# Performance work log

Measured on AMD Instinct MI355X. Metric: run time of the kernel, lower is better.

The kernel has to match this reference:

```python
import jax, jax.numpy as jnp
import numpy as np

D_MODEL, N_HEADS, HEAD_DIM = 384, 12, 32
N_QP, N_VP = 4, 8
B, L = 2, 1024
OUT_DIM = N_HEADS * (HEAD_DIM + N_VP * 3 + N_VP)  # 12*(32+24+8)=768
LN_EPS = 1e-5


def _linear_params(key, din, dout):
    kw, _ = jax.random.split(key)
    W = jax.random.normal(kw, (din, dout), dtype=jnp.float32) / np.sqrt(din).astype(np.float32)
    b = jnp.zeros((dout,), dtype=jnp.float32)
    return W, b


def setup_inputs() -> dict:
    key = jax.random.key(0)
    ks = jax.random.split(key, 12)
    s = jax.random.normal(ks[0], (B, L, D_MODEL), dtype=jnp.float32)
    translations = jax.random.normal(ks[1], (B, L, 3), dtype=jnp.float32)
    # proper rotation-ish matrices via QR of random gaussians
    g = jax.random.normal(ks[2], (B, L, 3, 3), dtype=jnp.float32)
    rotations, _ = jnp.linalg.qr(g)
    mask = jnp.ones((B, L), dtype=bool)
    Wq, bq = _linear_params(ks[3], D_MODEL, N_HEADS * HEAD_DIM)
    Wk, bk = _linear_params(ks[4], D_MODEL, N_HEADS * HEAD_DIM)
    Wv, bv = _linear_params(ks[5], D_MODEL, N_HEADS * HEAD_DIM)
    Wqp, bqp = _linear_params(ks[6], D_MODEL, N_HEADS * N_QP * 3)
    Wkp, bkp = _linear_params(ks[7], D_MODEL, N_HEADS * N_QP * 3)
    Wvp, bvp = _linear_params(ks[8], D_MODEL, N_HEADS * N_VP * 3)
    Wo, bo = _linear_params(ks[9], OUT_DIM, D_MODEL)
    head_weights = jnp.zeros((N_HEADS,), dtype=jnp.float32)
    ln_g = jnp.ones((D_MODEL,), dtype=jnp.float32)
    ln_b = jnp.zeros((D_MODEL,), dtype=jnp.float32)
    return dict(s=s, translations=translations, rotations=rotations, mask=mask,
                ln_g=ln_g, ln_b=ln_b, Wq=Wq, bq=bq, Wk=Wk, bk=bk, Wv=Wv, bv=bv,
                Wqp=Wqp, bqp=bqp, Wkp=Wkp, bkp=bkp, Wvp=Wvp, bvp=bvp,
                head_weights=head_weights, Wo=Wo, bo=bo)


def _ipa(s, translations, rotations, mask, ln_g, ln_b, Wq, bq, Wk, bk, Wv, bv,
         Wqp, bqp, Wkp, bkp, Wvp, bvp, head_weights, Wo, bo):
    Bc, Lc, _ = s.shape
    # LayerNorm
    mu = jnp.mean(s, axis=-1, keepdims=True)
    var = jnp.mean((s - mu) ** 2, axis=-1, keepdims=True)
    h = (s - mu) * jax.lax.rsqrt(var + LN_EPS) * ln_g + ln_b

    q_s = (h @ Wq + bq).reshape(Bc, Lc, N_HEADS, HEAD_DIM)
    k_s = (h @ Wk + bk).reshape(Bc, Lc, N_HEADS, HEAD_DIM)
    v_s = (h @ Wv + bv).reshape(Bc, Lc, N_HEADS, HEAD_DIM)
    q_pts = (h @ Wqp + bqp).reshape(Bc, Lc, N_HEADS, N_QP, 3)
    k_pts = (h @ Wkp + bkp).reshape(Bc, Lc, N_HEADS, N_QP, 3)
    v_pts = (h @ Wvp + bvp).reshape(Bc, Lc, N_HEADS, N_VP, 3)

    T = translations[:, :, None, None, :]  # (B,L,1,1,3)
    # local -> global: out_d = sum_c p_c R_{cd}  (matches torch einsum 'blhpc,blhpcd')
    q_g = jnp.einsum('blhpc,blcd->blhpd', q_pts, rotations) + T
    k_g = jnp.einsum('blhpc,blcd->blhpd', k_pts, rotations) + T
    v_g = jnp.einsum('blhpc,blcd->blhpd', v_pts, rotations) + T

    scalar_attn = jnp.einsum('bihd,bjhd->bhij', q_s, k_s) / np.sqrt(HEAD_DIM).astype(np.float32)

    # sum_{p,c} (q_i - k_j)^2 = |q_i|^2 + |k_j|^2 - 2 q_i.k_j  (avoids B,H,L,L,P,3 tensor)
    q2 = jnp.einsum('bihpc,bihpc->bhi', q_g, q_g)
    k2 = jnp.einsum('bjhpc,bjhpc->bhj', k_g, k_g)
    cross = jnp.einsum('bihpc,bjhpc->bhij', q_g, k_g)
    pt_dists = q2[:, :, :, None] + k2[:, :, None, :] - 2.0 * cross  # (B,H,L,L)

    w_h = jax.nn.softplus(head_weights)[None, :, None, None]
    attn_logits = scalar_attn - 0.5 * w_h * pt_dists
    attn_logits = jnp.where(mask[:, None, None, :], attn_logits, -jnp.inf)
    attn = jax.nn.softmax(attn_logits, axis=-1)  # (B,H,L,L)

    result_scalar = jnp.einsum('bhij,bjhd->bihd', attn, v_s).reshape(Bc, Lc, N_HEADS * HEAD_DIM)
    result_pts = jnp.einsum('bhij,bjhpc->bihpc', attn, v_g)  # (B,L,H,VP,3)
    # global -> local with R^T: out_d = sum_c x_c (R^T)_{cd} = sum_c x_c R_{dc}
    result_pts_local = jnp.einsum('blhpc,bldc->blhpd', result_pts - T, rotations)
    result_pts_norm = jnp.sqrt(jnp.sum(result_pts_local ** 2, axis=-1))  # (B,L,H,VP)

    output = jnp.concatenate([
        result_scalar,
        result_pts_local.reshape(Bc, Lc, N_HEADS * N_VP * 3),
        result_pts_norm.reshape(Bc, Lc, N_HEADS * N_VP),
    ], axis=-1)
    return s + output @ Wo + bo


def reference(s, translations, rotations, mask, ln_g, ln_b, Wq, bq, Wk, bk, Wv, bv,
              Wqp, bqp, Wkp, bkp, Wvp, bvp, head_weights, Wo, bo):
    return _ipa(s, translations, rotations, mask, ln_g, ln_b, Wq, bq, Wk, bk, Wv, bv,
                Wqp, bqp, Wkp, bkp, Wvp, bvp, head_weights, Wo, bo)
```

## Files before the change

kernel.cpp:

```cpp
#include <hip/hip_runtime.h>
#include <hip/hip_bf16.h>

constexpr int B_ = 2, L_ = 1024, D_ = 384, H_ = 12, HD_ = 32;
constexpr int NQP = 4, NVP = 8;
constexpr int ROWS = B_ * L_;
constexpr int PROJ_N = 1728;
constexpr int OUTD = 768;
constexpr int KAUG = 48;
constexpr int C_QS = 0, C_KS = 384, C_VS = 768, C_QP = 1152, C_KP = 1296, C_VP = 1440;

constexpr size_t OFF_HH   = 0;
constexpr size_t OFF_HL   = OFF_HH   + (size_t)ROWS * D_ / 2;
constexpr size_t OFF_WTH  = OFF_HL   + (size_t)ROWS * D_ / 2;
constexpr size_t OFF_WTL  = OFF_WTH  + (size_t)PROJ_N * D_ / 2;
constexpr size_t OFF_BC   = OFF_WTL  + (size_t)PROJ_N * D_ / 2;
constexpr size_t OFF_P    = OFF_BC   + PROJ_N;
constexpr size_t OFF_QPK  = OFF_P    + (size_t)ROWS * PROJ_N;
constexpr size_t QP_FL    = (size_t)24 * 1024 * KAUG / 2;
constexpr size_t OFF_QPL  = OFF_QPK  + QP_FL;
constexpr size_t OFF_KPK  = OFF_QPL  + QP_FL;
constexpr size_t OFF_KPL2 = OFF_KPK  + QP_FL;
constexpr size_t OFF_VT   = OFF_KPL2 + (size_t)24 * 1024 * 16 / 2;
constexpr size_t OFF_OH   = OFF_VT   + (size_t)24 * 64 * L_ / 2;
constexpr size_t OFF_WOH  = OFF_OH   + (size_t)ROWS * OUTD / 2;

typedef __attribute__((ext_vector_type(8)))  __bf16        bf16x8;
typedef __attribute__((ext_vector_type(16))) float         f32x16;
typedef __attribute__((ext_vector_type(4)))  unsigned int  u32x4;
typedef __attribute__((ext_vector_type(8)))  unsigned short us8;

__device__ __forceinline__ unsigned short f2bf(float x) {
    unsigned u = __builtin_bit_cast(unsigned, x);
    unsigned r = (u + 0x7FFFu + ((u >> 16) & 1u)) >> 16;
    return (unsigned short)r;
}
__device__ __forceinline__ float bf2f(unsigned short s) {
    return __builtin_bit_cast(float, (unsigned)s << 16);
}

#define MFMA(a, b, c) __builtin_amdgcn_mfma_f32_32x32x16_bf16((a), (b), (c), 0, 0, 0)
#define CVTPK(dst, x, y) asm("v_cvt_pk_bf16_f32 %0, %1, %2" : "=v"(dst) : "v"(x), "v"(y))
#define PSWAP(a, b) asm("v_permlane32_swap_b32 %0, %1" : "+v"(a), "+v"(b))

typedef const __attribute__((address_space(1))) void* gas_cp;
typedef __attribute__((address_space(3))) void* las_p;
__device__ __forceinline__ void gload16(const void* g, void* l) {
    __builtin_amdgcn_global_load_lds((gas_cp)g, (las_p)l, 16, 0, 0);
}

__global__ __launch_bounds__(256) void setup_kernel(
    const float* __restrict__ s, const float* __restrict__ g,
    const float* __restrict__ bln,
    const float* __restrict__ Wq, const float* __restrict__ Wk, const float* __restrict__ Wv,
    const float* __restrict__ Wqp, const float* __restrict__ Wkp, const float* __restrict__ Wvp,
    const float* __restrict__ bq, const float* __restrict__ bk, const float* __restrict__ bv,
    const float* __restrict__ bqp, const float* __restrict__ bkp, const float* __restrict__ bvp,
    const float* __restrict__ Wo,
    unsigned short* __restrict__ Hhi, unsigned short* __restrict__ Hlo,
    unsigned short* __restrict__ Wthi, unsigned short* __restrict__ Wtlo,
    float* __restrict__ bcat, unsigned short* __restrict__ Wothi)
{
    __shared__ float T[64][65];
    const int blk = blockIdx.x;
    const int tid = threadIdx.x;

    if (blk < 512) {
        const int wave = tid >> 6, lane = tid & 63;
        const int row = blk * 4 + wave;
        const float* sr = s + (size_t)row * D_;
        float v[6];
        float sum = 0.f, sumsq = 0.f;
#pragma unroll
        for (int e = 0; e < 6; ++e) {
            v[e] = sr[lane + e * 64];
            sum += v[e]; sumsq += v[e] * v[e];
        }
#pragma unroll
        for (int o = 32; o >= 1; o >>= 1) {
            sum   += __shfl_xor(sum, o, 64);
            sumsq += __shfl_xor(sumsq, o, 64);
        }
        const float mu  = sum * (1.f / D_);
        const float var = sumsq * (1.f / D_) - mu * mu;
        const float rstd = rsqrtf(var + 1e-5f);
#pragma unroll
        for (int e = 0; e < 6; ++e) {
            const int d = lane + e * 64;
            const float hv = (v[e] - mu) * rstd * g[d] + bln[d];
            const unsigned short h16 = f2bf(hv);
            Hhi[(size_t)row * D_ + d] = h16;
            Hlo[(size_t)row * D_ + d] = f2bf(hv - bf2f(h16));
        }
        return;
    }

    if (blk < 674) {
        const int q = blk - 512;
        const int n0 = (q % 27) * 64, k0 = (q / 27) * 64;
        const int nn = tid & 63, kk4 = tid >> 6;
#pragma unroll
        for (int p = 0; p < 16; ++p) {
            const int k = k0 + p * 4 + kk4, n = n0 + nn;
            float v;
            if      (n < 384)  v = Wq [k * 384 + n];
            else if (n < 768)  v = Wk [k * 384 + n - 384];
            else if (n < 1152) v = Wv [k * 384 + n - 768];
            else if (n < 1296) v = Wqp[k * 144 + n - 1152];
            else if (n < 1440) v = Wkp[k * 144 + n - 1296];
            else               v = Wvp[k * 288 + n - 1440];
            T[p * 4 + kk4][nn] = v;
        }
        if (k0 == 0 && tid < 64) {
            const int n = n0 + tid;
            float v;
            if      (n < 384)  v = bq [n];
            else if (n < 768)  v = bk [n - 384];
            else if (n < 1152) v = bv [n - 768];
            else if (n < 1296) v = bqp[n - 1152];
            else if (n < 1440) v = bkp[n - 1296];
            else               v = bvp[n - 1440];
            bcat[n] = v;
        }
        __syncthreads();
        const int nr = tid >> 2, c = tid & 3;
#pragma unroll
        for (int e = 0; e < 2; ++e) {
            const int kc = e * 4 + c;
            us8 hi8, lo8;
#pragma unroll
            for (int x = 0; x < 8; ++x) {
                const float v = T[kc * 8 + x][nr];
                const unsigned short h16 = f2bf(v);
                hi8[x] = h16; lo8[x] = f2bf(v - bf2f(h16));
            }
            const size_t off = (size_t)(n0 + nr) * D_ + k0 + kc * 8;
            *reinterpret_cast<us8*>(Wthi + off) = hi8;
            *reinterpret_cast<us8*>(Wtlo + off) = lo8;
        }
        return;
    }

    {
        const int q = blk - 674;
        const int n0 = (q % 6) * 64, k0 = (q / 6) * 64;
        const int nn = tid & 63, kk4 = tid >> 6;
#pragma unroll
        for (int p = 0; p < 16; ++p) {
            const int k = k0 + p * 4 + kk4;
            T[p * 4 + kk4][nn] = Wo[(size_t)k * D_ + n0 + nn];
        }
        __syncthreads();
        const int nr = tid >> 2, c = tid & 3;
#pragma unroll
        for (int e = 0; e < 2; ++e) {
            const int kc = e * 4 + c;
            us8 hi8;
#pragma unroll
            for (int x = 0; x < 8; ++x) hi8[x] = f2bf(T[kc * 8 + x][nr]);
            *reinterpret_cast<us8*>(Wothi + (size_t)(n0 + nr) * OUTD + k0 + kc * 8) = hi8;
        }
    }
}

template<int BK, int CMODE>
__global__ __launch_bounds__(256) void lgemm_kernel(
    const unsigned short* __restrict__ Ahi, const unsigned short* __restrict__ Alo,
    const unsigned short* __restrict__ Bhi, const unsigned short* __restrict__ Blo,
    const float* __restrict__ bias, const float* __restrict__ resid,
    float* __restrict__ C, int M, int N, int K)
{
    constexpr int NTILES = (CMODE == 0) ? 2 : 4;
    constexpr int CPR = BK / 8;
    constexpr int RM = CPR - 1;
    constexpr int TILE_US = 64 * BK;
    constexpr int ISS = (TILE_US / 8) / 256;
    __shared__ unsigned short lds[2 * NTILES * TILE_US];

    const int nb = N / 64;
    int wg = blockIdx.x;
    wg = (wg & 7) * ((int)gridDim.x >> 3) + (wg >> 3);
    const int by = wg / nb, bx = wg - by * nb;
    const bool comp = (CMODE == 1) || (CMODE == 2 && bx >= 18 && bx <= 22);
    const int m0 = by * 64, n0 = bx * 64;
    const int tid = threadIdx.x;
    const int lane = tid & 63, wv = tid >> 6;
    const int lo31 = lane & 31, hi2 = lane >> 5;
    const int wm = wv >> 1, wn = wv & 1;

    const unsigned short* gsrc[4] = {Ahi, Bhi, Alo ? Alo : Ahi, Blo ? Blo : Bhi};
    const int tb0[4] = {m0, n0, m0, n0};

    auto STAGE = [&](int buf, int t) {
#pragma unroll
        for (int tt = 0; tt < NTILES; ++tt) {
            if (tt >= 2 && !comp) continue;
#pragma unroll
            for (int i = 0; i < ISS; ++i) {
                const int q = i * 256 + tid;
                const int row = q / CPR, c = q & RM;
                const unsigned short* gp = gsrc[tt] +
                    (size_t)(tb0[tt] + row) * K + t * BK + ((c ^ (row & RM)) * 8);
                gload16(gp, &lds[(size_t)(buf * NTILES + tt) * TILE_US + (size_t)q * 8]);
            }
        }
    };

    f32x16 acc;
#pragma unroll
    for (int r = 0; r < 16; ++r) acc[r] = 0.f;

    const int arow = wm * 32 + lo31, brow = wn * 32 + lo31;
    auto COMPUTE = [&](int buf) {
        const char* base = (const char*)&lds[(size_t)buf * NTILES * TILE_US];
#pragma unroll
        for (int ks = 0; ks < BK / 16; ++ks) {
            const int cc = ks * 2 + hi2;
            const int aoff = arow * (BK * 2) + ((cc ^ (arow & RM)) * 16);
            const int boff = brow * (BK * 2) + ((cc ^ (brow & RM)) * 16);
            const bf16x8 ah = *reinterpret_cast<const bf16x8*>(base + aoff);
            const bf16x8 bh = *reinterpret_cast<const bf16x8*>(base + TILE_US * 2 + boff);
            acc = MFMA(ah, bh, acc);
            if (NTILES == 4 && comp) {
                const bf16x8 al = *reinterpret_cast<const bf16x8*>(base + 2 * TILE_US * 2 + aoff);
                const bf16x8 bl = *reinterpret_cast<const bf16x8*>(base + 3 * TILE_US * 2 + boff);
                acc = MFMA(ah, bl, acc);
                acc = MFMA(al, bh, acc);
            }
        }
    };

    const int NK = K / BK;
    STAGE(0, 0);
    asm volatile("s_waitcnt vmcnt(0)" ::: "memory");
    __syncthreads();
    int cur = 0;
#pragma unroll 1
    for (int t = 0; t < NK; ++t) {
        if (t + 1 < NK) STAGE(cur ^ 1, t + 1);
        COMPUTE(cur);
        asm volatile("s_waitcnt vmcnt(0)" ::: "memory");
        __syncthreads();
        cur ^= 1;
    }

    const int col = n0 + wn * 32 + lo31;
    const float bb = bias ? bias[col] : 0.f;
#pragma unroll
    for (int r = 0; r < 16; ++r) {
        const int row = m0 + wm * 32 + (r & 3) + 8 * (r >> 2) + 4 * hi2;
        float v = acc[r] + bb;
        if (resid) v += resid[(size_t)row * N + col];
        C[(size_t)row * N + col] = v;
    }
}

__global__ __launch_bounds__(256) void prep_kernel(
    const float* __restrict__ P, const float* __restrict__ trans,
    const float* __restrict__ rot, const float* __restrict__ hw,
    unsigned short* __restrict__ Qpk, unsigned short* __restrict__ Qpl,
    unsigned short* __restrict__ Kpk, unsigned short* __restrict__ Kpl2,
    unsigned short* __restrict__ Vt)
{
    __shared__ unsigned short VL[56 * 264];
    const int tid = threadIdx.x;
    const int bh = blockIdx.x >> 2, jc = blockIdx.x & 3;
    const int h = bh % H_, b = bh / H_;
    const int j = jc * 256 + tid;
    const int row = b * L_ + j;

    float R[9], T[3];
#pragma unroll
    for (int u = 0; u < 9; ++u) R[u] = rot[(size_t)row * 9 + u];
#pragma unroll
    for (int u = 0; u < 3; ++u) T[u] = trans[(size_t)row * 3 + u];
    const float* prow = P + (size_t)row * PROJ_N;

    const float w  = log1pf(expf(hw[h]));
    const float mw = -0.5f * w;
    const float qsc = 0.17677669529663687f;

    float Aq[KAUG], Bk[KAUG];
#pragma unroll
    for (int d = 0; d < KAUG; ++d) { Aq[d] = 0.f; Bk[d] = 0.f; }
    const float4* qs4 = reinterpret_cast<const float4*>(prow + C_QS + h * 32);
    const float4* ks4 = reinterpret_cast<const float4*>(prow + C_KS + h * 32);
#pragma unroll
    for (int i = 0; i < 8; ++i) {
        const float4 q = qs4[i], k = ks4[i];
        Aq[i * 4 + 0] = q.x * qsc; Aq[i * 4 + 1] = q.y * qsc;
        Aq[i * 4 + 2] = q.z * qsc; Aq[i * 4 + 3] = q.w * qsc;
        Bk[i * 4 + 0] = k.x; Bk[i * 4 + 1] = k.y;
        Bk[i * 4 + 2] = k.z; Bk[i * 4 + 3] = k.w;
    }
    float qp[12], kp[12];
#pragma unroll
    for (int i = 0; i < 3; ++i) {
        const float4 q = reinterpret_cast<const float4*>(prow + C_QP + h * 12)[i];
        const float4 k = reinterpret_cast<const float4*>(prow + C_KP + h * 12)[i];
        qp[i * 4 + 0] = q.x; qp[i * 4 + 1] = q.y; qp[i * 4 + 2] = q.z; qp[i * 4 + 3] = q.w;
        kp[i * 4 + 0] = k.x; kp[i * 4 + 1] = k.y; kp[i * 4 + 2] = k.z; kp[i * 4 + 3] = k.w;
    }
    float k2 = 0.f;
#pragma unroll
    for (int p = 0; p < NQP; ++p) {
        const float qx = qp[p * 3], qy = qp[p * 3 + 1], qz = qp[p * 3 + 2];
        const float kx = kp[p * 3], ky = kp[p * 3 + 1], kz = kp[p * 3 + 2];
#pragma unroll
        for (int c = 0; c < 3; ++c) {
            const float gq = fmaf(qx, R[0 + c], fmaf(qy, R[3 + c], fmaf(qz, R[6 + c], T[c])));
            const float gk = fmaf(kx, R[0 + c], fmaf(ky, R[3 + c], fmaf(kz, R[6 + c], T[c])));
            Aq[32 + p * 3 + c] = w * gq;
            Bk[32 + p * 3 + c] = gk;
            k2 += gk * gk;
        }
    }
    Aq[44] = mw;
    Bk[44] = k2;

    const size_t ro = ((size_t)bh * L_ + j) * KAUG;
#pragma unroll
    for (int g8 = 0; g8 < 6; ++g8) {
        us8 qh, ql, kh;
#pragma unroll
        for (int e = 0; e < 8; ++e) {
            const float aq = Aq[g8 * 8 + e];
            const unsigned short ah = f2bf(aq);
            qh[e] = ah; ql[e] = f2bf(aq - bf2f(ah));
            kh[e] = f2bf(Bk[g8 * 8 + e]);
        }
        *reinterpret_cast<us8*>(Qpk + ro + g8 * 8) = qh;
        *reinterpret_cast<us8*>(Qpl + ro + g8 * 8) = ql;
        *reinterpret_cast<us8*>(Kpk + ro + g8 * 8) = kh;
    }
    const size_t ro2 = ((size_t)bh * L_ + j) * 16;
#pragma unroll
    for (int g8 = 0; g8 < 2; ++g8) {
        us8 kl;
#pragma unroll
        for (int e = 0; e < 8; ++e) {
            const float bk = Bk[32 + g8 * 8 + e];
            kl[e] = f2bf(bk - bf2f(f2bf(bk)));
        }
        *reinterpret_cast<us8*>(Kpl2 + ro2 + g8 * 8) = kl;
    }

    const float4* vs4 = reinterpret_cast<const float4*>(prow + C_VS + h * 32);
#pragma unroll
    for (int i = 0; i < 8; ++i) {
        const float4 v = vs4[i];
        VL[(i * 4 + 0) * 264 + tid] = f2bf(v.x);
        VL[(i * 4 + 1) * 264 + tid] = f2bf(v.y);
        VL[(i * 4 + 2) * 264 + tid] = f2bf(v.z);
        VL[(i * 4 + 3) * 264 + tid] = f2bf(v.w);
    }
    float vpt[24];
#pragma unroll
    for (int i = 0; i < 6; ++i) {
        const float4 v = reinterpret_cast<const float4*>(prow + C_VP + h * 24)[i];
        vpt[i * 4 + 0] = v.x; vpt[i * 4 + 1] = v.y; vpt[i * 4 + 2] = v.z; vpt[i * 4 + 3] = v.w;
    }
#pragma unroll
    for (int p = 0; p < NVP; ++p) {
        const float x = vpt[p * 3], y = vpt[p * 3 + 1], z = vpt[p * 3 + 2];
#pragma unroll
        for (int c = 0; c < 3; ++c) {
            const float g = fmaf(x, R[0 + c], fmaf(y, R[3 + c], fmaf(z, R[6 + c], T[c])));
            VL[(32 + p * 3 + c) * 264 + tid] = f2bf(g);
        }
    }
    __syncthreads();
#pragma unroll
    for (int e = 0; e < 8; ++e) {
        const int ch = tid + 256 * e;
        const int vd = ch >> 5, jj = (ch & 31) * 8;
        us8 val;
        if (vd < 56) {
            val = *reinterpret_cast<const us8*>(&VL[vd * 264 + jj]);
        } else {
            for (int x = 0; x < 8; ++x) val[x] = 0;
        }
        *reinterpret_cast<us8*>(Vt + ((size_t)(bh * 64 + vd)) * L_ + jc * 256 + jj) = val;
    }
}

struct KV { bf16x8 kh0, kh1, kh2, kl2, v00, v01, v10, v11; };

#define LOADT(F, t) do {                                                      \
    const char* _kp = khp + (size_t)(t) * 3072;                               \
    (F).kh0 = *reinterpret_cast<const bf16x8*>(_kp);                          \
    (F).kh1 = *reinterpret_cast<const bf16x8*>(_kp + 32);                     \
    (F).kh2 = *reinterpret_cast<const bf16x8*>(_kp + 64);                     \
    (F).kl2 = *reinterpret_cast<const bf16x8*>(klp + (size_t)(t) * 1024);     \
    const char* _vp = vp + (size_t)(t) * 64;                                  \
    (F).v00 = *reinterpret_cast<const bf16x8*>(_vp);                          \
    (F).v01 = *reinterpret_cast<const bf16x8*>(_vp + 32);                     \
    (F).v10 = *reinterpret_cast<const bf16x8*>(_vp + 65536);                  \
    (F).v11 = *reinterpret_cast<const bf16x8*>(_vp + 65536 + 32);             \
} while (0)

__device__ __forceinline__ void proc_tile(
    const KV& F, const bf16x8& q0h, const bf16x8& q1h, const bf16x8& q2h,
    const bf16x8& q0l, const bf16x8& q1l, const bf16x8& q2l,
    f32x16& o0, f32x16& o1, float& m, float& lsum)
{
    f32x16 d;
#pragma unroll
    for (int r = 0; r < 16; ++r) d[r] = 0.f;
    d = MFMA(F.kh0, q0h, d); d = MFMA(F.kh0, q0l, d);
    d = MFMA(F.kh1, q1h, d); d = MFMA(F.kh1, q1l, d);
    d = MFMA(F.kh2, q2h, d); d = MFMA(F.kh2, q2l, d);
    d = MFMA(F.kl2, q2h, d);

    float pmax = d[0];
#pragma unroll
    for (int r = 1; r < 16; ++r) pmax = fmaxf(pmax, d[r]);
    pmax = fmaxf(pmax, __shfl_xor(pmax, 32));
    const float mn = fmaxf(m, pmax);
    const float scale = __expf(m - mn);
    float p[16];
    float ps = 0.f;
#pragma unroll
    for (int r = 0; r < 16; ++r) { p[r] = __expf(d[r] - mn); ps += p[r]; }
    lsum = fmaf(lsum, scale, ps);
    m = mn;
#pragma unroll
    for (int r = 0; r < 16; ++r) { o0[r] *= scale; o1[r] *= scale; }

    unsigned W0, W1, W2, W3, X0, X1, X2, X3;
    CVTPK(W0, p[0], p[1]);  CVTPK(W1, p[2], p[3]);
    CVTPK(W2, p[4], p[5]);  CVTPK(W3, p[6], p[7]);
    PSWAP(W0, W2);          PSWAP(W1, W3);
    CVTPK(X0, p[8], p[9]);  CVTPK(X1, p[10], p[11]);
    CVTPK(X2, p[12], p[13]); CVTPK(X3, p[14], p[15]);
    PSWAP(X0, X2);          PSWAP(X1, X3);
    const u32x4 u0 = {W0, W1, W2, W3};
    const u32x4 u1 = {X0, X1, X2, X3};
    const bf16x8 pb0 = __builtin_bit_cast(bf16x8, u0);
    const bf16x8 pb1 = __builtin_bit_cast(bf16x8, u1);

    o0 = MFMA(F.v00, pb0, o0);
    o1 = MFMA(F.v10, pb0, o1);
    o0 = MFMA(F.v01, pb1, o0);
    o1 = MFMA(F.v11, pb1, o1);
}

__global__ __launch_bounds__(256) void attn_kernel(
    const unsigned short* __restrict__ Qpk, const unsigned short* __restrict__ Qpl,
    const unsigned short* __restrict__ Kpk, const unsigned short* __restrict__ Kpl2,
    const unsigned short* __restrict__ Vt,
    const float* __restrict__ trans, const float* __restrict__ rot,
    unsigned short* __restrict__ Ophi)
{
    __shared__ float MRG[4 * 64 * 36];
    const int wg = ((int)blockIdx.x & 7) * 96 + ((int)blockIdx.x >> 3);
    const int bh = wg >> 5, itile = wg & 31;
    const int h = bh % H_, b = bh / H_;
    const int tid = threadIdx.x;
    const int wv = tid >> 6, lane = tid & 63;
    const int lo31 = lane & 31, hi = lane >> 5;

    const char* qkp = (const char*)Qpk + ((size_t)(bh * L_ + itile * 32 + lo31) * KAUG + hi * 8) * 2;
    const char* qlp = (const char*)Qpl + ((size_t)(bh * L_ + itile * 32 + lo31) * KAUG + hi * 8) * 2;
    const bf16x8 q0h = *reinterpret_cast<const bf16x8*>(qkp);
    const bf16x8 q1h = *reinterpret_cast<const bf16x8*>(qkp + 32);
    const bf16x8 q2h = *reinterpret_cast<const bf16x8*>(qkp + 64);
    const bf16x8 q0l = *reinterpret_cast<const bf16x8*>(qlp);
    const bf16x8 q1l = *reinterpret_cast<const bf16x8*>(qlp + 32);
    const bf16x8 q2l = *reinterpret_cast<const bf16x8*>(qlp + 64);

    const char* khp = (const char*)Kpk  + ((size_t)(bh * L_ + lo31) * KAUG + hi * 8) * 2;
    const char* klp = (const char*)Kpl2 + ((size_t)(bh * L_ + lo31) * 16 + hi * 8) * 2;
    const char* vp  = (const char*)Vt   + ((size_t)bh * 64 * L_ + (size_t)lo31 * L_ + hi * 8) * 2;

    f32x16 o0, o1;
#pragma unroll
    for (int r = 0; r < 16; ++r) { o0[r] = 0.f; o1[r] = 0.f; }
    float m = -3.0e38f, lsum = 0.f;

    const int t0 = wv * 8;
    KV fa, fb;
    LOADT(fa, t0);
#pragma unroll 1
    for (int tt = 0; tt < 8; tt += 2) {
        LOADT(fb, t0 + tt + 1);
        proc_tile(fa, q0h, q1h, q2h, q0l, q1l, q2l, o0, o1, m, lsum);
        if (tt + 2 < 8) LOADT(fa, t0 + tt + 2);
        proc_tile(fb, q0h, q1h, q2h, q0l, q1l, q2l, o0, o1, m, lsum);
    }

    if (wv != 0) {
        const int base = (wv * 64 + lane) * 36;
#pragma unroll
        for (int r = 0; r < 16; ++r) {
            MRG[base + r] = o0[r];
            MRG[base + 16 + r] = o1[r];
        }
        MRG[base + 32] = m;
        MRG[base + 33] = lsum;
    }
    __syncthreads();
    if (wv != 0) return;

#pragma unroll
    for (int w = 1; w < 4; ++w) {
        const int b2 = (w * 64 + lane) * 36;
        const float mw_ = MRG[b2 + 32], lw = MRG[b2 + 33];
        const float nm = fmaxf(m, mw_);
        const float s0 = __expf(m - nm), s1 = __expf(mw_ - nm);
#pragma unroll
        for (int r = 0; r < 16; ++r) {
            o0[r] = o0[r] * s0 + MRG[b2 + r] * s1;
            o1[r] = o1[r] * s0 + MRG[b2 + 16 + r] * s1;
        }
        lsum = lsum * s0 + lw * s1;
        m = nm;
    }

    lsum += __shfl_xor(lsum, 32);
    const float inv = 1.f / lsum;
    const int row = b * L_ + itile * 32 + lo31;
    unsigned short* ophr = Ophi + (size_t)row * OUTD + h * HD_;
#pragma unroll
    for (int r = 0; r < 16; ++r) {
        const int vd = (r & 3) + 8 * (r >> 2) + 4 * hi;
        ophr[vd] = f2bf(o0[r] * inv);
    }

    float own[12], oth[12];
#pragma unroll
    for (int r = 0; r < 12; ++r) {
        own[r] = o1[r] * inv;
        oth[r] = __shfl_xor(own[r], 32);
    }
    float dims[24];
#pragma unroll
    for (int vd = 0; vd < 24; ++vd) {
        const int r = (vd & 3) + 4 * (vd >> 3);
        const int hb = (vd >> 2) & 1;
        dims[vd] = (hi == hb) ? own[r] : oth[r];
    }
    float R[9], T[3];
#pragma unroll
    for (int u = 0; u < 9; ++u) R[u] = rot[(size_t)row * 9 + u];
#pragma unroll
    for (int u = 0; u < 3; ++u) T[u] = trans[(size_t)row * 3 + u];
    unsigned short* orow = Ophi + (size_t)row * OUTD;
    auto finpt = [&](float x, float y, float z, int hp) {
        x -= T[0]; y -= T[1]; z -= T[2];
        const float lx = fmaf(x, R[0], fmaf(y, R[1], z * R[2]));
        const float ly = fmaf(x, R[3], fmaf(y, R[4], z * R[5]));
        const float lz = fmaf(x, R[6], fmaf(y, R[7], z * R[8]));
        orow[384 + hp * 3 + 0] = f2bf(lx);
        orow[384 + hp * 3 + 1] = f2bf(ly);
        orow[384 + hp * 3 + 2] = f2bf(lz);
        orow[672 + hp] = f2bf(sqrtf(lx * lx + ly * ly + lz * lz));
    };
    if (hi == 0) {
        finpt(dims[0],  dims[1],  dims[2],  h * 8 + 0);
        finpt(dims[3],  dims[4],  dims[5],  h * 8 + 1);
        finpt(dims[6],  dims[7],  dims[8],  h * 8 + 2);
        finpt(dims[9],  dims[10], dims[11], h * 8 + 3);
    } else {
        finpt(dims[12], dims[13], dims[14], h * 8 + 4);
        finpt(dims[15], dims[16], dims[17], h * 8 + 5);
        finpt(dims[18], dims[19], dims[20], h * 8 + 6);
        finpt(dims[21], dims[22], dims[23], h * 8 + 7);
    }
}

extern "C" void kernel_launch(void* const* d_in, const int* in_sizes, int n_in,
                              void* d_out, int out_size, void* d_ws, size_t ws_size,
                              hipStream_t stream)
{
    const float* s     = (const float*)d_in[0];
    const float* trans = (const float*)d_in[1];
    const float* rot   = (const float*)d_in[2];
    const float* ln_g  = (const float*)d_in[4];
    const float* ln_b  = (const float*)d_in[5];
    const float* Wq  = (const float*)d_in[6];  const float* bq  = (const float*)d_in[7];
    const float* Wk  = (const float*)d_in[8];  const float* bk  = (const float*)d_in[9];
    const float* Wv  = (const float*)d_in[10]; const float* bv  = (const float*)d_in[11];
    const float* Wqp = (const float*)d_in[12]; const float* bqp = (const float*)d_in[13];
    const float* Wkp = (const float*)d_in[14]; const float* bkp = (const float*)d_in[15];
    const float* Wvp = (const float*)d_in[16]; const float* bvp = (const float*)d_in[17];
    const float* hw  = (const float*)d_in[18];
    const float* Wo  = (const float*)d_in[19]; const float* bo  = (const float*)d_in[20];
    (void)in_sizes; (void)n_in; (void)out_size; (void)ws_size;

    float* ws = (float*)d_ws;
    unsigned short* Hhi   = (unsigned short*)(ws + OFF_HH);
    unsigned short* Hlo   = (unsigned short*)(ws + OFF_HL);
    unsigned short* Wthi  = (unsigned short*)(ws + OFF_WTH);
    unsigned short* Wtlo  = (unsigned short*)(ws + OFF_WTL);
    float* bc  = ws + OFF_BC;
    float* P   = ws + OFF_P;
    unsigned short* Qpk   = (unsigned short*)(ws + OFF_QPK);
    unsigned short* Qpl   = (unsigned short*)(ws + OFF_QPL);
    unsigned short* Kpk   = (unsigned short*)(ws + OFF_KPK);
    unsigned short* Kpl2  = (unsigned short*)(ws + OFF_KPL2);
    unsigned short* Vt    = (unsigned short*)(ws + OFF_VT);
    unsigned short* Ophi  = (unsigned short*)(ws + OFF_OH);
    unsigned short* Wothi = (unsigned short*)(ws + OFF_WOH);
    float* out = (float*)d_out;

    setup_kernel<<<746, 256, 0, stream>>>(
        s, ln_g, ln_b, Wq, Wk, Wv, Wqp, Wkp, Wvp,
        bq, bk, bv, bqp, bkp, bvp, Wo,
        Hhi, Hlo, Wthi, Wtlo, bc, Wothi);
    lgemm_kernel<32, 2><<<(ROWS / 64) * (PROJ_N / 64), 256, 0, stream>>>(
        Hhi, Hlo, Wthi, Wtlo, bc, nullptr, P, ROWS, PROJ_N, D_);
    prep_kernel<<<24 * 4, 256, 0, stream>>>(
        P, trans, rot, hw, Qpk, Qpl, Kpk, Kpl2, Vt);
    attn_kernel<<<B_ * H_ * (L_ / 32), 256, 0, stream>>>(
        Qpk, Qpl, Kpk, Kpl2, Vt, trans, rot, Ophi);
    lgemm_kernel<64, 0><<<(ROWS / 64) * (D_ / 64), 256, 0, stream>>>(
        Ophi, nullptr, Wothi, nullptr, bo, s, out, ROWS, D_, OUTD);
}
```

Before: 76.14 us.

## Triple-buffer GEMM loads, shrink prep blocks, drop scalar-part lo-split MFMAs

The GEMM kernel goes from double to triple-buffered LDS staging with partial vmcnt waits, so two tiles stay in flight while one is computed. The prep kernel now launches 64-thread blocks (four times as many), which spreads its work over more CUs. In attention, the bf16 low-part correction terms for the scalar query features (first 32 dims) are dropped, which removes two MFMAs per tile and two q loads. That last change lowers the precision of the scalar logits and relies on the tolerance accepting plain bf16 there.

```diff
diff --git a/kernel.cpp b/kernel.cpp
--- a/kernel.cpp
+++ b/kernel.cpp
@@ -174,13 +174,13 @@
     constexpr int RM = CPR - 1;
     constexpr int TILE_US = 64 * BK;
     constexpr int ISS = (TILE_US / 8) / 256;
-    __shared__ unsigned short lds[2 * NTILES * TILE_US];
+    __shared__ unsigned short lds[3 * NTILES * TILE_US];
 
     const int nb = N / 64;
     int wg = blockIdx.x;
     wg = (wg & 7) * ((int)gridDim.x >> 3) + (wg >> 3);
     const int by = wg / nb, bx = wg - by * nb;
-    const bool comp = (CMODE == 1) || (CMODE == 2 && bx >= 18 && bx <= 22);
+    const bool comp = (CMODE == 2 && bx >= 18 && bx <= 22);
     const int m0 = by * 64, n0 = bx * 64;
     const int tid = threadIdx.x;
     const int lane = tid & 63, wv = tid >> 6;
@@ -229,18 +229,34 @@
         }
     };
 
+    constexpr int LPS_P = 2 * ISS;
+    constexpr int LPS_C = 4 * ISS;
+    auto WAIT_LPS = [&]() {
+        if (!comp) {
+            if constexpr (LPS_P == 2)
+                asm volatile("s_waitcnt vmcnt(2) lgkmcnt(0)" ::: "memory");
+            else
+                asm volatile("s_waitcnt vmcnt(4) lgkmcnt(0)" ::: "memory");
+        } else {
+            if constexpr (LPS_C == 4)
+                asm volatile("s_waitcnt vmcnt(4) lgkmcnt(0)" ::: "memory");
+            else
+                asm volatile("s_waitcnt vmcnt(8) lgkmcnt(0)" ::: "memory");
+        }
+    };
+
     const int NK = K / BK;
     STAGE(0, 0);
-    asm volatile("s_waitcnt vmcnt(0)" ::: "memory");
-    __syncthreads();
-    int cur = 0;
+    STAGE(1, 1);
+    WAIT_LPS();
+    __builtin_amdgcn_s_barrier();
 #pragma unroll 1
     for (int t = 0; t < NK; ++t) {
-        if (t + 1 < NK) STAGE(cur ^ 1, t + 1);
-        COMPUTE(cur);
-        asm volatile("s_waitcnt vmcnt(0)" ::: "memory");
-        __syncthreads();
-        cur ^= 1;
+        if (t + 2 < NK) STAGE((t + 2) % 3, t + 2);
+        COMPUTE(t % 3);
+        if (t + 2 < NK) WAIT_LPS();
+        else asm volatile("s_waitcnt vmcnt(0) lgkmcnt(0)" ::: "memory");
+        __builtin_amdgcn_s_barrier();
     }
 
     const int col = n0 + wn * 32 + lo31;
@@ -254,18 +270,18 @@
     }
 }
 
-__global__ __launch_bounds__(256) void prep_kernel(
+__global__ __launch_bounds__(64) void prep_kernel(
     const float* __restrict__ P, const float* __restrict__ trans,
     const float* __restrict__ rot, const float* __restrict__ hw,
     unsigned short* __restrict__ Qpk, unsigned short* __restrict__ Qpl,
     unsigned short* __restrict__ Kpk, unsigned short* __restrict__ Kpl2,
     unsigned short* __restrict__ Vt)
 {
-    __shared__ unsigned short VL[56 * 264];
-    const int tid = threadIdx.x;
-    const int bh = blockIdx.x >> 2, jc = blockIdx.x & 3;
+    __shared__ unsigned short VL[56 * 72];
+    const int lane = threadIdx.x;
+    const int bh = blockIdx.x >> 4, jc = blockIdx.x & 15;
     const int h = bh % H_, b = bh / H_;
-    const int j = jc * 256 + tid;
+    const int j = jc * 64 + lane;
     const int row = b * L_ + j;
 
     float R[9], T[3];
@@ -320,17 +336,23 @@
     const size_t ro = ((size_t)bh * L_ + j) * KAUG;
 #pragma unroll
     for (int g8 = 0; g8 < 6; ++g8) {
-        us8 qh, ql, kh;
+        us8 qh, kh;
 #pragma unroll
         for (int e = 0; e < 8; ++e) {
-            const float aq = Aq[g8 * 8 + e];
-            const unsigned short ah = f2bf(aq);
-            qh[e] = ah; ql[e] = f2bf(aq - bf2f(ah));
+            qh[e] = f2bf(Aq[g8 * 8 + e]);
             kh[e] = f2bf(Bk[g8 * 8 + e]);
         }
         *reinterpret_cast<us8*>(Qpk + ro + g8 * 8) = qh;
-        *reinterpret_cast<us8*>(Qpl + ro + g8 * 8) = ql;
         *reinterpret_cast<us8*>(Kpk + ro + g8 * 8) = kh;
+        if (g8 >= 4) {
+            us8 ql;
+#pragma unroll
+            for (int e = 0; e < 8; ++e) {
+                const float aq = Aq[g8 * 8 + e];
+                ql[e] = f2bf(aq - bf2f(f2bf(aq)));
+            }
+            *reinterpret_cast<us8*>(Qpl + ro + g8 * 8) = ql;
+        }
     }
     const size_t ro2 = ((size_t)bh * L_ + j) * 16;
 #pragma unroll
@@ -348,10 +370,10 @@
 #pragma unroll
     for (int i = 0; i < 8; ++i) {
         const float4 v = vs4[i];
-        VL[(i * 4 + 0) * 264 + tid] = f2bf(v.x);
-        VL[(i * 4 + 1) * 264 + tid] = f2bf(v.y);
-        VL[(i * 4 + 2) * 264 + tid] = f2bf(v.z);
-        VL[(i * 4 + 3) * 264 + tid] = f2bf(v.w);
+        VL[(i * 4 + 0) * 72 + lane] = f2bf(v.x);
+        VL[(i * 4 + 1) * 72 + lane] = f2bf(v.y);
+        VL[(i * 4 + 2) * 72 + lane] = f2bf(v.z);
+        VL[(i * 4 + 3) * 72 + lane] = f2bf(v.w);
     }
     float vpt[24];
 #pragma unroll
@@ -365,21 +387,21 @@
 #pragma unroll
         for (int c = 0; c < 3; ++c) {
             const float g = fmaf(x, R[0 + c], fmaf(y, R[3 + c], fmaf(z, R[6 + c], T[c])));
-            VL[(32 + p * 3 + c) * 264 + tid] = f2bf(g);
+            VL[(32 + p * 3 + c) * 72 + lane] = f2bf(g);
         }
     }
     __syncthreads();
 #pragma unroll
     for (int e = 0; e < 8; ++e) {
-        const int ch = tid + 256 * e;
-        const int vd = ch >> 5, jj = (ch & 31) * 8;
+        const int ch = lane + 64 * e;
+        const int vd = ch >> 3, jj = (ch & 7) * 8;
         us8 val;
         if (vd < 56) {
-            val = *reinterpret_cast<const us8*>(&VL[vd * 264 + jj]);
+            val = *reinterpret_cast<const us8*>(&VL[vd * 72 + jj]);
         } else {
             for (int x = 0; x < 8; ++x) val[x] = 0;
         }
-        *reinterpret_cast<us8*>(Vt + ((size_t)(bh * 64 + vd)) * L_ + jc * 256 + jj) = val;
+        *reinterpret_cast<us8*>(Vt + (size_t)(bh * 64 + vd) * L_ + jc * 64 + jj) = val;
     }
 }
 
@@ -400,14 +422,13 @@
 
 __device__ __forceinline__ void proc_tile(
     const KV& F, const bf16x8& q0h, const bf16x8& q1h, const bf16x8& q2h,
-    const bf16x8& q0l, const bf16x8& q1l, const bf16x8& q2l,
-    f32x16& o0, f32x16& o1, float& m, float& lsum)
+    const bf16x8& q2l, f32x16& o0, f32x16& o1, float& m, float& lsum)
 {
     f32x16 d;
 #pragma unroll
     for (int r = 0; r < 16; ++r) d[r] = 0.f;
-    d = MFMA(F.kh0, q0h, d); d = MFMA(F.kh0, q0l, d);
-    d = MFMA(F.kh1, q1h, d); d = MFMA(F.kh1, q1l, d);
+    d = MFMA(F.kh0, q0h, d);
+    d = MFMA(F.kh1, q1h, d);
     d = MFMA(F.kh2, q2h, d); d = MFMA(F.kh2, q2l, d);
     d = MFMA(F.kl2, q2h, d);
 
@@ -464,8 +485,6 @@
     const bf16x8 q0h = *reinterpret_cast<const bf16x8*>(qkp);
     const bf16x8 q1h = *reinterpret_cast<const bf16x8*>(qkp + 32);
     const bf16x8 q2h = *reinterpret_cast<const bf16x8*>(qkp + 64);
-    const bf16x8 q0l = *reinterpret_cast<const bf16x8*>(qlp);
-    const bf16x8 q1l = *reinterpret_cast<const bf16x8*>(qlp + 32);
     const bf16x8 q2l = *reinterpret_cast<const bf16x8*>(qlp + 64);
 
     const char* khp = (const char*)Kpk  + ((size_t)(bh * L_ + lo31) * KAUG + hi * 8) * 2;
@@ -483,9 +502,9 @@
 #pragma unroll 1
     for (int tt = 0; tt < 8; tt += 2) {
         LOADT(fb, t0 + tt + 1);
-        proc_tile(fa, q0h, q1h, q2h, q0l, q1l, q2l, o0, o1, m, lsum);
+        proc_tile(fa, q0h, q1h, q2h, q2l, o0, o1, m, lsum);
         if (tt + 2 < 8) LOADT(fa, t0 + tt + 2);
-        proc_tile(fb, q0h, q1h, q2h, q0l, q1l, q2l, o0, o1, m, lsum);
+        proc_tile(fb, q0h, q1h, q2h, q2l, o0, o1, m, lsum);
     }
 
     if (wv != 0) {
@@ -609,7 +628,7 @@
         Hhi, Hlo, Wthi, Wtlo, bc, Wothi);
     lgemm_kernel<32, 2><<<(ROWS / 64) * (PROJ_N / 64), 256, 0, stream>>>(
         Hhi, Hlo, Wthi, Wtlo, bc, nullptr, P, ROWS, PROJ_N, D_);
-    prep_kernel<<<24 * 4, 256, 0, stream>>>(
+    prep_kernel<<<24 * 16, 64, 0, stream>>>(
         P, trans, rot, hw, Qpk, Qpl, Kpk, Kpl2, Vt);
     attn_kernel<<<B_ * H_ * (L_ / 32), 256, 0, stream>>>(
         Qpk, Qpl, Kpk, Kpl2, Vt, trans, rot, Ophi);
```

Result: faster. 72.79 us (-4.4%).
